# Performance work log

Measured on AMD Instinct MI355X. Metric: run time of the kernel, lower is better.

## Reference

```python
import jax, jax.numpy as jnp
import numpy as np

N = 50000
E = 800000
IN_CH = 128
HID = 64
OUT_CH = 40
NUM_LAYERS = 8
ALPHA = 0.1
THETA = 0.5


def setup_inputs() -> dict:
    key = jax.random.key(0)
    ks = jax.random.split(key, 10)
    x = jax.random.normal(ks[0], (N, IN_CH), dtype=jnp.float32)
    edge_src = jax.random.randint(ks[1], (E,), 0, N, dtype=jnp.int32)
    edge_dst = jax.random.randint(ks[2], (E,), 0, N, dtype=jnp.int32)
    edge_weight = jax.random.uniform(ks[3], (E,), dtype=jnp.float32)
    # parameters
    W_in = jax.random.normal(ks[4], (IN_CH, HID), dtype=jnp.float32) / np.sqrt(IN_CH)
    b_in = jnp.zeros((HID,), dtype=jnp.float32)
    W_convs = jax.random.normal(ks[5], (NUM_LAYERS, HID, HID), dtype=jnp.float32) / np.sqrt(HID)
    W_out = jax.random.normal(ks[6], (HID, OUT_CH), dtype=jnp.float32) / np.sqrt(HID)
    b_out = jnp.zeros((OUT_CH,), dtype=jnp.float32)
    return {"x": x, "edge_src": edge_src, "edge_dst": edge_dst,
            "edge_weight": edge_weight, "W_in": W_in, "b_in": b_in,
            "W_convs": W_convs, "W_out": W_out, "b_out": b_out}


def _spmm(edge_src, edge_dst, edge_weight, h):
    # adj_t @ h : gather source features, scale by edge weight, scatter-add to dst
    msg = h[edge_src] * edge_weight[:, None]          # [E, HID]
    return jax.ops.segment_sum(msg, edge_dst, num_segments=N)


def reference(x, edge_src, edge_dst, edge_weight, W_in, b_in, W_convs, W_out, b_out):
    # entry linear + relu (dropout=0 -> identity)
    x0 = jax.nn.relu(x @ W_in + b_in)                 # [N, HID]
    h = x0
    for l in range(NUM_LAYERS):
        beta = float(np.log(THETA / (l + 1) + 1.0))
        agg = _spmm(edge_src, edge_dst, edge_weight, h)
        u = (1.0 - ALPHA) * agg + ALPHA * x0          # initial-residual blend
        out = (1.0 - beta) * u + beta * (u @ W_convs[l])  # identity-mapped weight
        h = jax.nn.relu(out)
    return h @ W_out + b_out                          # [N, OUT_CH]
```

## Files before the change

kernel.cpp:

```cpp
#include <hip/hip_runtime.h>
#include <math.h>

#define NN 50000
#define EE 800000
#define INCH 128
#define HID 64
#define OUTCH 40
#define NUM_LAYERS 8
#define CAP 64

__device__ __forceinline__ float frelu(float v) { return v > 0.f ? v : 0.f; }

__device__ __forceinline__ unsigned int f2bf(float f) {
  unsigned int u = __float_as_uint(f);
  return (u + 0x7fffu + ((u >> 16) & 1u)) >> 16;
}
__device__ __forceinline__ float bf_lo(unsigned int v) { return __uint_as_float(v << 16); }
__device__ __forceinline__ float bf_hi(unsigned int v) { return __uint_as_float(v & 0xffff0000u); }

__global__ __launch_bounds__(256) void entry_gemm(
    const float* __restrict__ x, const float* __restrict__ W,
    const float* __restrict__ b, unsigned int* __restrict__ x0h) {
  __shared__ float Wl[INCH * HID];
  __shared__ float xT[INCH][68];
  __shared__ float bl[HID];
  const int t = threadIdx.x;
  const int base = blockIdx.x * 64;

  #pragma unroll
  for (int i = 0; i < 8; ++i) {
    const int f4 = i * 256 + t;
    *(float4*)&Wl[f4 * 4] = *(const float4*)&W[f4 * 4];
  }
  if (t < HID) bl[t] = b[t];
  #pragma unroll
  for (int i = 0; i < 8; ++i) {
    const int f4 = i * 256 + t;
    const int row = f4 >> 5;
    const int col = (f4 & 31) * 4;
    float4 v = make_float4(0.f, 0.f, 0.f, 0.f);
    if (base + row < NN) v = *(const float4*)&x[(size_t)(base + row) * INCH + col];
    xT[col + 0][row] = v.x; xT[col + 1][row] = v.y;
    xT[col + 2][row] = v.z; xT[col + 3][row] = v.w;
  }
  __syncthreads();

  const int r0 = (t >> 4) * 4;
  const int c0 = (t & 15) * 4;
  float acc[4][4] = {};
  #pragma unroll 4
  for (int k = 0; k < INCH; ++k) {
    const float4 a = *(const float4*)&xT[k][r0];
    const float4 wv = *(const float4*)&Wl[k * HID + c0];
    const float av[4] = {a.x, a.y, a.z, a.w};
    const float wvv[4] = {wv.x, wv.y, wv.z, wv.w};
    #pragma unroll
    for (int i = 0; i < 4; ++i)
      #pragma unroll
      for (int j = 0; j < 4; ++j) acc[i][j] += av[i] * wvv[j];
  }

  #pragma unroll
  for (int i = 0; i < 4; ++i) {
    const int row = base + r0 + i;
    if (row < NN) {
      const float o0 = frelu(acc[i][0] + bl[c0 + 0]);
      const float o1 = frelu(acc[i][1] + bl[c0 + 1]);
      const float o2 = frelu(acc[i][2] + bl[c0 + 2]);
      const float o3 = frelu(acc[i][3] + bl[c0 + 3]);
      uint2 pw;
      pw.x = f2bf(o0) | (f2bf(o1) << 16);
      pw.y = f2bf(o2) | (f2bf(o3) << 16);
      *(uint2*)&x0h[(size_t)row * 32 + (c0 >> 1)] = pw;
    }
  }
}

__global__ __launch_bounds__(256) void scatter_build(
    const int* __restrict__ src, const int* __restrict__ dst,
    const float* __restrict__ w, int* __restrict__ counts,
    unsigned int* __restrict__ edges4) {
  const int i = blockIdx.x * 256 + threadIdx.x;
  if (i < EE) {
    const int d = dst[i];
    const int pos = atomicAdd(&counts[d], 1);
    if (pos < CAP) {
      const unsigned int w15 = (unsigned int)rintf(w[i] * 32767.f);
      edges4[(size_t)d * CAP + pos] = ((unsigned int)src[i] << 15) | w15;
    }
  }
}

__global__ __launch_bounds__(256) void layer_fused(
    const int* __restrict__ counts, const unsigned int* __restrict__ edges4,
    const unsigned int* __restrict__ hin, const unsigned int* __restrict__ x0h,
    const float* __restrict__ W, float beta, unsigned int* __restrict__ hout) {
  __shared__ float Wl[HID * HID];
  __shared__ float uT[32][68];
  const int t = threadIdx.x;
  const int g = t >> 3;
  const int li = t & 7;
  const int gb = (t & 63) & 56;
  const int node = blockIdx.x * 32 + g;
  const float wscale = 1.f / 32767.f;
  const uint4* hrows = (const uint4*)hin;

  #pragma unroll
  for (int i = 0; i < 4; ++i) {
    const int f4 = i * 256 + t;
    *(float4*)&Wl[f4 * 4] = *(const float4*)&W[f4 * 4];
  }

  float a[8] = {0.f, 0.f, 0.f, 0.f, 0.f, 0.f, 0.f, 0.f};
  if (node < NN) {
    const int deg = min(counts[node], CAP);
    const int be = node * CAP;
    for (int e0 = 0; e0 < deg; e0 += 8) {
      const unsigned int ev = edges4[be + e0 + li];
      unsigned int e_[8];
      uint4 h_[8];
      float w_[8];
      #pragma unroll
      for (int m = 0; m < 8; ++m) e_[m] = __shfl(ev, gb + m);
      #pragma unroll
      for (int m = 0; m < 8; ++m) {
        h_[m] = hrows[(size_t)(e_[m] >> 15) * 8 + li];
        w_[m] = (float)(e_[m] & 32767u) * wscale;
      }
      #pragma unroll
      for (int m = 0; m < 8; ++m) {
        a[0] += w_[m] * bf_lo(h_[m].x); a[1] += w_[m] * bf_hi(h_[m].x);
        a[2] += w_[m] * bf_lo(h_[m].y); a[3] += w_[m] * bf_hi(h_[m].y);
        a[4] += w_[m] * bf_lo(h_[m].z); a[5] += w_[m] * bf_hi(h_[m].z);
        a[6] += w_[m] * bf_lo(h_[m].w); a[7] += w_[m] * bf_hi(h_[m].w);
      }
    }
    const uint4 xq = ((const uint4*)x0h)[(size_t)node * 8 + li];
    float4 uA, uB;
    uA.x = 0.9f * a[0] + 0.1f * bf_lo(xq.x);
    uA.y = 0.9f * a[1] + 0.1f * bf_hi(xq.x);
    uA.z = 0.9f * a[2] + 0.1f * bf_lo(xq.y);
    uA.w = 0.9f * a[3] + 0.1f * bf_hi(xq.y);
    uB.x = 0.9f * a[4] + 0.1f * bf_lo(xq.z);
    uB.y = 0.9f * a[5] + 0.1f * bf_hi(xq.z);
    uB.z = 0.9f * a[6] + 0.1f * bf_lo(xq.w);
    uB.w = 0.9f * a[7] + 0.1f * bf_hi(xq.w);
    *(float4*)&uT[g][8 * li + 0] = uA;
    *(float4*)&uT[g][8 * li + 4] = uB;
  }
  __syncthreads();

  const int r0 = (t >> 4) * 2;
  const int c0 = (t & 15) * 4;
  float acc[2][4] = {};
  #pragma unroll 4
  for (int k = 0; k < HID; ++k) {
    const float u0 = uT[r0 + 0][k];
    const float u1 = uT[r0 + 1][k];
    const float4 wq = *(const float4*)&Wl[k * HID + c0];
    acc[0][0] += u0 * wq.x; acc[0][1] += u0 * wq.y;
    acc[0][2] += u0 * wq.z; acc[0][3] += u0 * wq.w;
    acc[1][0] += u1 * wq.x; acc[1][1] += u1 * wq.y;
    acc[1][2] += u1 * wq.z; acc[1][3] += u1 * wq.w;
  }

  const float omb = 1.f - beta;
  #pragma unroll
  for (int i = 0; i < 2; ++i) {
    const int row = blockIdx.x * 32 + r0 + i;
    if (row < NN) {
      const float4 uq = *(const float4*)&uT[r0 + i][c0];
      const float o0 = frelu(omb * uq.x + beta * acc[i][0]);
      const float o1 = frelu(omb * uq.y + beta * acc[i][1]);
      const float o2 = frelu(omb * uq.z + beta * acc[i][2]);
      const float o3 = frelu(omb * uq.w + beta * acc[i][3]);
      uint2 pw;
      pw.x = f2bf(o0) | (f2bf(o1) << 16);
      pw.y = f2bf(o2) | (f2bf(o3) << 16);
      *(uint2*)&hout[(size_t)row * 32 + (c0 >> 1)] = pw;
    }
  }
}

__global__ __launch_bounds__(256) void out_gemm(
    const unsigned int* __restrict__ hp, const float* __restrict__ W,
    const float* __restrict__ b, float* __restrict__ out) {
  __shared__ float hl[64][65];
  __shared__ float Wl[HID * OUTCH];
  __shared__ float bl[OUTCH];
  const int t = threadIdx.x;
  const int base = blockIdx.x * 64;

  #pragma unroll
  for (int i = 0; i < 8; ++i) {
    const int idx = i * 256 + t;
    const int row = idx >> 5;
    const int c = idx & 31;
    unsigned int v = 0;
    if (base + row < NN) v = hp[(size_t)(base + row) * 32 + c];
    hl[row][2 * c + 0] = bf_lo(v);
    hl[row][2 * c + 1] = bf_hi(v);
  }
  for (int i = t; i < HID * OUTCH; i += 256) Wl[i] = W[i];
  if (t < OUTCH) bl[t] = b[t];
  __syncthreads();

  const int r = t & 63;
  const int g = t >> 6;
  const int c0 = g * 10;
  float acc[10] = {};
  for (int k = 0; k < HID; ++k) {
    const float hv = hl[r][k];
    #pragma unroll
    for (int j = 0; j < 10; ++j) acc[j] += hv * Wl[k * OUTCH + c0 + j];
  }
  const int row = base + r;
  if (row < NN) {
    #pragma unroll
    for (int j = 0; j < 10; ++j) out[(size_t)row * OUTCH + c0 + j] = acc[j] + bl[c0 + j];
  }
}

extern "C" void kernel_launch(void* const* d_in, const int* in_sizes, int n_in,
                              void* d_out, int out_size, void* d_ws, size_t ws_size,
                              hipStream_t stream) {
  const float* x     = (const float*)d_in[0];
  const int* esrc    = (const int*)d_in[1];
  const int* edst    = (const int*)d_in[2];
  const float* ew    = (const float*)d_in[3];
  const float* W_in  = (const float*)d_in[4];
  const float* b_in  = (const float*)d_in[5];
  const float* W_cv  = (const float*)d_in[6];
  const float* W_out = (const float*)d_in[7];
  const float* b_out = (const float*)d_in[8];
  float* out = (float*)d_out;

  char* w = (char*)d_ws;
  unsigned int* x0h    = (unsigned int*)(w + 0);
  unsigned int* hA     = (unsigned int*)(w + 6400000);
  unsigned int* hB     = (unsigned int*)(w + 12800000);
  int* counts          = (int*)(w + 19200000);
  unsigned int* edges4 = (unsigned int*)(w + 19400064);

  const int gemm_grid  = (NN + 63) / 64;
  const int edge_grid  = (EE + 255) / 256;
  const int layer_grid = (NN + 31) / 32;

  entry_gemm<<<gemm_grid, 256, 0, stream>>>(x, W_in, b_in, x0h);

  hipMemsetAsync(counts, 0, NN * sizeof(int), stream);
  hipMemsetAsync(edges4, 0, (size_t)NN * CAP * sizeof(unsigned int), stream);
  scatter_build<<<edge_grid, 256, 0, stream>>>(esrc, edst, ew, counts, edges4);

  const unsigned int* hin = x0h;
  unsigned int* hcur = hA;
  for (int l = 0; l < NUM_LAYERS; ++l) {
    const float beta = logf(0.5f / (float)(l + 1) + 1.0f);
    layer_fused<<<layer_grid, 256, 0, stream>>>(counts, edges4, hin, x0h,
                                                W_cv + (size_t)l * HID * HID,
                                                beta, hcur);
    hin = hcur;
    hcur = (hcur == hA) ? hB : hA;
  }

  out_gemm<<<gemm_grid, 256, 0, stream>>>((const unsigned int*)hin, W_out, b_out, out);
}
```

Baseline: 265.2 us.

## Sort nodes by degree for layer load balance and prefetch edge chunks

After: 524.2 us. 97.6% more time.

```diff
diff --git a/kernel.cpp b/kernel.cpp
--- a/kernel.cpp
+++ b/kernel.cpp
@@ -91,7 +91,40 @@
   }
 }
 
+__global__ __launch_bounds__(256) void deg_hist(const int* __restrict__ counts,
+                                                int* __restrict__ dbins) {
+  const int n = blockIdx.x * 256 + threadIdx.x;
+  if (n < NN) atomicAdd(&dbins[min(counts[n], CAP)], 1);
+}
+
+__global__ __launch_bounds__(128) void deg_scan(int* __restrict__ dbins) {
+  __shared__ int s[2][128];
+  const int t = threadIdx.x;
+  const int v = (t < CAP + 1) ? dbins[t] : 0;
+  int p = 0;
+  s[0][t] = v;
+  __syncthreads();
+  for (int off = 1; off < 128; off <<= 1) {
+    s[p ^ 1][t] = s[p][t] + ((t >= off) ? s[p][t - off] : 0);
+    p ^= 1;
+    __syncthreads();
+  }
+  if (t < CAP + 1) dbins[t] = s[p][t] - v;
+}
+
+__global__ __launch_bounds__(256) void perm_build(const int* __restrict__ counts,
+                                                  int* __restrict__ dbins,
+                                                  int* __restrict__ perm) {
+  const int n = blockIdx.x * 256 + threadIdx.x;
+  if (n < NN) {
+    const int d = min(counts[n], CAP);
+    const int pos = atomicAdd(&dbins[d], 1);
+    perm[pos] = n;
+  }
+}
+
 __global__ __launch_bounds__(256) void layer_fused(
+    const int* __restrict__ perm,
     const int* __restrict__ counts, const unsigned int* __restrict__ edges4,
     const unsigned int* __restrict__ hin, const unsigned int* __restrict__ x0h,
     const float* __restrict__ W, float beta, unsigned int* __restrict__ hout) {
@@ -101,7 +134,7 @@
   const int g = t >> 3;
   const int li = t & 7;
   const int gb = (t & 63) & 56;
-  const int node = blockIdx.x * 32 + g;
+  const int node = perm[blockIdx.x * 32 + g];
   const float wscale = 1.f / 32767.f;
   const uint4* hrows = (const uint4*)hin;
 
@@ -112,11 +145,12 @@
   }
 
   float a[8] = {0.f, 0.f, 0.f, 0.f, 0.f, 0.f, 0.f, 0.f};
-  if (node < NN) {
+  {
     const int deg = min(counts[node], CAP);
     const int be = node * CAP;
+    unsigned int ev = (deg > 0) ? edges4[be + li] : 0u;
     for (int e0 = 0; e0 < deg; e0 += 8) {
-      const unsigned int ev = edges4[be + e0 + li];
+      const unsigned int evn = (e0 + 8 < deg) ? edges4[be + e0 + 8 + li] : 0u;
       unsigned int e_[8];
       uint4 h_[8];
       float w_[8];
@@ -134,6 +168,7 @@
         a[4] += w_[m] * bf_lo(h_[m].z); a[5] += w_[m] * bf_hi(h_[m].z);
         a[6] += w_[m] * bf_lo(h_[m].w); a[7] += w_[m] * bf_hi(h_[m].w);
       }
+      ev = evn;
     }
     const uint4 xq = ((const uint4*)x0h)[(size_t)node * 8 + li];
     float4 uA, uB;
@@ -167,18 +202,16 @@
   const float omb = 1.f - beta;
   #pragma unroll
   for (int i = 0; i < 2; ++i) {
-    const int row = blockIdx.x * 32 + r0 + i;
-    if (row < NN) {
-      const float4 uq = *(const float4*)&uT[r0 + i][c0];
-      const float o0 = frelu(omb * uq.x + beta * acc[i][0]);
-      const float o1 = frelu(omb * uq.y + beta * acc[i][1]);
-      const float o2 = frelu(omb * uq.z + beta * acc[i][2]);
-      const float o3 = frelu(omb * uq.w + beta * acc[i][3]);
-      uint2 pw;
-      pw.x = f2bf(o0) | (f2bf(o1) << 16);
-      pw.y = f2bf(o2) | (f2bf(o3) << 16);
-      *(uint2*)&hout[(size_t)row * 32 + (c0 >> 1)] = pw;
-    }
+    const int rnode = perm[blockIdx.x * 32 + r0 + i];
+    const float4 uq = *(const float4*)&uT[r0 + i][c0];
+    const float o0 = frelu(omb * uq.x + beta * acc[i][0]);
+    const float o1 = frelu(omb * uq.y + beta * acc[i][1]);
+    const float o2 = frelu(omb * uq.z + beta * acc[i][2]);
+    const float o3 = frelu(omb * uq.w + beta * acc[i][3]);
+    uint2 pw;
+    pw.x = f2bf(o0) | (f2bf(o1) << 16);
+    pw.y = f2bf(o2) | (f2bf(o3) << 16);
+    *(uint2*)&hout[(size_t)rnode * 32 + (c0 >> 1)] = pw;
   }
 }
 
@@ -240,23 +273,32 @@
   unsigned int* hA     = (unsigned int*)(w + 6400000);
   unsigned int* hB     = (unsigned int*)(w + 12800000);
   int* counts          = (int*)(w + 19200000);
-  unsigned int* edges4 = (unsigned int*)(w + 19400064);
+  int* perm            = (int*)(w + 19400064);
+  int* dbins           = (int*)(w + 19600256);
+  unsigned int* edges4 = (unsigned int*)(w + 19600768);
 
   const int gemm_grid  = (NN + 63) / 64;
   const int edge_grid  = (EE + 255) / 256;
+  const int node_grid  = (NN + 255) / 256;
   const int layer_grid = (NN + 31) / 32;
 
   entry_gemm<<<gemm_grid, 256, 0, stream>>>(x, W_in, b_in, x0h);
 
   hipMemsetAsync(counts, 0, NN * sizeof(int), stream);
   hipMemsetAsync(edges4, 0, (size_t)NN * CAP * sizeof(unsigned int), stream);
+  hipMemsetAsync(dbins, 0, (CAP + 1) * sizeof(int), stream);
+  hipMemsetAsync(perm + NN, 0, (size_t)(layer_grid * 32 - NN) * sizeof(int), stream);
+
   scatter_build<<<edge_grid, 256, 0, stream>>>(esrc, edst, ew, counts, edges4);
+  deg_hist<<<node_grid, 256, 0, stream>>>(counts, dbins);
+  deg_scan<<<1, 128, 0, stream>>>(dbins);
+  perm_build<<<node_grid, 256, 0, stream>>>(counts, dbins, perm);
 
   const unsigned int* hin = x0h;
   unsigned int* hcur = hA;
   for (int l = 0; l < NUM_LAYERS; ++l) {
     const float beta = logf(0.5f / (float)(l + 1) + 1.0f);
-    layer_fused<<<layer_grid, 256, 0, stream>>>(counts, edges4, hin, x0h,
+    layer_fused<<<layer_grid, 256, 0, stream>>>(perm, counts, edges4, hin, x0h,
                                                 W_cv + (size_t)l * HID * HID,
                                                 beta, hcur);
     hin = hcur;
```

## Replace global-atomic edge scatter with two-pass bucketed counting sort

Applied to the files above, without the earlier changes.

Result: faster. 250.7 us (-5.5%).

```diff
diff --git a/kernel.cpp b/kernel.cpp
--- a/kernel.cpp
+++ b/kernel.cpp
@@ -8,6 +8,10 @@
 #define OUTCH 40
 #define NUM_LAYERS 8
 #define CAP 64
+
+#define EPB 4096
+#define NBLK 196
+#define NBKT 196
 
 __device__ __forceinline__ float frelu(float v) { return v > 0.f ? v : 0.f; }
 
@@ -76,19 +80,98 @@
   }
 }
 
-__global__ __launch_bounds__(256) void scatter_build(
+__global__ __launch_bounds__(256) void edge_hist(const int* __restrict__ dst,
+                                                 int* __restrict__ cnt) {
+  __shared__ int hist[256];
+  const int t = threadIdx.x;
+  hist[t] = 0;
+  __syncthreads();
+  const int e0 = blockIdx.x * EPB;
+  #pragma unroll
+  for (int i = 0; i < 16; ++i) {
+    const int e = e0 + i * 256 + t;
+    if (e < EE) atomicAdd(&hist[dst[e] >> 8], 1);
+  }
+  __syncthreads();
+  cnt[t * 200 + blockIdx.x] = hist[t];
+}
+
+__global__ __launch_bounds__(256) void scan_cnt(int* __restrict__ cnt,
+                                                int* __restrict__ tot) {
+  __shared__ int s[2][256];
+  const int t = threadIdx.x;
+  const int b = blockIdx.x;
+  const int v = (t < NBLK) ? cnt[b * 200 + t] : 0;
+  int p = 0;
+  s[0][t] = v;
+  __syncthreads();
+  for (int off = 1; off < 256; off <<= 1) {
+    s[p ^ 1][t] = s[p][t] + ((t >= off) ? s[p][t - off] : 0);
+    p ^= 1;
+    __syncthreads();
+  }
+  if (t < NBLK) cnt[b * 200 + t] = s[p][t] - v;
+  if (t == 255) tot[b] = s[p][255];
+}
+
+__global__ __launch_bounds__(256) void scan_tot(const int* __restrict__ tot,
+                                                int* __restrict__ base) {
+  __shared__ int s[2][256];
+  const int t = threadIdx.x;
+  const int v = (t < NBKT) ? tot[t] : 0;
+  int p = 0;
+  s[0][t] = v;
+  __syncthreads();
+  for (int off = 1; off < 256; off <<= 1) {
+    s[p ^ 1][t] = s[p][t] + ((t >= off) ? s[p][t - off] : 0);
+    p ^= 1;
+    __syncthreads();
+  }
+  base[t] = s[p][t] - v;
+}
+
+__global__ __launch_bounds__(256) void edge_place(
     const int* __restrict__ src, const int* __restrict__ dst,
-    const float* __restrict__ w, int* __restrict__ counts,
-    unsigned int* __restrict__ edges4) {
-  const int i = blockIdx.x * 256 + threadIdx.x;
-  if (i < EE) {
-    const int d = dst[i];
-    const int pos = atomicAdd(&counts[d], 1);
-    if (pos < CAP) {
-      const unsigned int w15 = (unsigned int)rintf(w[i] * 32767.f);
-      edges4[(size_t)d * CAP + pos] = ((unsigned int)src[i] << 15) | w15;
+    const float* __restrict__ w, const int* __restrict__ cnt,
+    const int* __restrict__ base, uint2* __restrict__ buf8) {
+  __shared__ int cur[256];
+  const int t = threadIdx.x;
+  cur[t] = (t < NBKT) ? (base[t] + cnt[t * 200 + blockIdx.x]) : 0;
+  __syncthreads();
+  const int e0 = blockIdx.x * EPB;
+  #pragma unroll
+  for (int i = 0; i < 16; ++i) {
+    const int e = e0 + i * 256 + t;
+    if (e < EE) {
+      const int d = dst[e];
+      const int pos = atomicAdd(&cur[d >> 8], 1);
+      const unsigned int w15 = (unsigned int)rintf(w[e] * 32767.f);
+      buf8[pos] = make_uint2(((unsigned int)src[e] << 15) | w15,
+                             (unsigned int)(d & 255));
     }
   }
+}
+
+__global__ __launch_bounds__(256) void bucket_place(
+    const int* __restrict__ base, const int* __restrict__ tot,
+    const uint2* __restrict__ buf8, unsigned int* __restrict__ edges4,
+    int* __restrict__ counts) {
+  __shared__ int cur2[256];
+  const int t = threadIdx.x;
+  const int b = blockIdx.x;
+  cur2[t] = 0;
+  __syncthreads();
+  const int start = base[b];
+  const int n = tot[b];
+  for (int i = t; i < n; i += 256) {
+    const uint2 rec = buf8[start + i];
+    const int pos = atomicAdd(&cur2[rec.y], 1);
+    if (pos < CAP)
+      edges4[(size_t)((b << 8) + rec.y) * CAP + pos] = rec.x;
+  }
+  __syncthreads();
+  const int node = (b << 8) + t;
+  if (node < NN) counts[node] = min(cur2[t], CAP);
 }
 
 __global__ __launch_bounds__(256) void layer_fused(
@@ -113,7 +196,7 @@
 
   float a[8] = {0.f, 0.f, 0.f, 0.f, 0.f, 0.f, 0.f, 0.f};
   if (node < NN) {
-    const int deg = min(counts[node], CAP);
+    const int deg = counts[node];
     const int be = node * CAP;
     for (int e0 = 0; e0 < deg; e0 += 8) {
       const unsigned int ev = edges4[be + e0 + li];
@@ -240,17 +323,23 @@
   unsigned int* hA     = (unsigned int*)(w + 6400000);
   unsigned int* hB     = (unsigned int*)(w + 12800000);
   int* counts          = (int*)(w + 19200000);
-  unsigned int* edges4 = (unsigned int*)(w + 19400064);
+  int* cnt             = (int*)(w + 19400064);
+  int* tot             = (int*)(w + 19604864);
+  int* base            = (int*)(w + 19605888);
+  uint2* buf8          = (uint2*)(w + 19606912);
+  unsigned int* edges4 = (unsigned int*)(w + 26006912);
 
   const int gemm_grid  = (NN + 63) / 64;
-  const int edge_grid  = (EE + 255) / 256;
   const int layer_grid = (NN + 31) / 32;
 
   entry_gemm<<<gemm_grid, 256, 0, stream>>>(x, W_in, b_in, x0h);
 
-  hipMemsetAsync(counts, 0, NN * sizeof(int), stream);
   hipMemsetAsync(edges4, 0, (size_t)NN * CAP * sizeof(unsigned int), stream);
-  scatter_build<<<edge_grid, 256, 0, stream>>>(esrc, edst, ew, counts, edges4);
+  edge_hist<<<NBLK, 256, 0, stream>>>(edst, cnt);
+  scan_cnt<<<NBKT, 256, 0, stream>>>(cnt, tot);
+  scan_tot<<<1, 256, 0, stream>>>(tot, base);
+  edge_place<<<NBLK, 256, 0, stream>>>(esrc, edst, ew, cnt, base, buf8);
+  bucket_place<<<NBKT, 256, 0, stream>>>(base, tot, buf8, edges4, counts);
 
   const unsigned int* hin = x0h;
   unsigned int* hcur = hA;
```
